# Optimization experiments

Hardware: AMD Instinct MI355X
Metric: run time of the kernel (lower is better)

The kernel has to match this reference:

```python
import jax, jax.numpy as jnp
import numpy as np

M, N, K = 1024, 11008, 4096


def _unpack_i2u(Bp):
    """Unpack 2-bit unsigned weights per decode_i2u_to_i8s interleave.

    Bp: [N, K//4] int8 storage. Within each group of 4 bytes (16 elements),
    output element at position 4*i + j = (byte_j >> (2*i)) & 3.
    Returns [N, K] int8 with values in {0,1,2,3}.
    """
    Bu = jax.lax.bitcast_convert_type(Bp, jnp.uint8)  # [N, K//4]
    n, kc = Bu.shape
    Bg = Bu.reshape(n, kc // 4, 1, 4)                 # [N, G, 1, j]
    shifts = (jnp.arange(4, dtype=jnp.uint8) * jnp.uint8(2)).reshape(1, 1, 4, 1)
    vals = (Bg >> shifts) & jnp.uint8(3)              # [N, G, i, j]
    return vals.reshape(n, kc * 4).astype(jnp.int8)   # [N, K]


def setup_inputs() -> dict:
    key = jax.random.key(0)
    k1, k2 = jax.random.split(key)
    A = jax.random.randint(k1, (M, K), -128, 128, dtype=jnp.int8)
    B = jax.random.randint(k2, (N, K // 4), -128, 128, dtype=jnp.int8)
    return {"A": A, "B": B}


def reference(A, B):
    W = _unpack_i2u(B)  # [N, K] int8
    C = jax.lax.dot_general(
        A, W,
        dimension_numbers=(((1,), (1,)), ((), ())),
        preferred_element_type=jnp.int32,
    )  # [M, N] int32
    return C
```

## Files before the change

### kernel.cpp

```cpp
#include <hip/hip_runtime.h>
#include <stdint.h>


#define MM 1024
#define NN 11008
#define KK 4096
#define MTILES 8
#define NTILES 86
#define NBLOCKS (MTILES * NTILES)
#define STRIDE_A ((size_t)MTILES * 8192)
#define STRIDE_B ((size_t)NTILES * 2048)

using i32x4  = __attribute__((ext_vector_type(4))) int;
using i32x16 = __attribute__((ext_vector_type(16))) int;

__device__ __forceinline__ int pack4(i32x4 v) {
    return (int)(((uint32_t)v[0] & 0xFFu) | (((uint32_t)v[1] & 0xFFu) << 8)
               | (((uint32_t)v[2] & 0xFFu) << 16) | (((uint32_t)v[3] & 0xFFu) << 24));
}

__global__ __launch_bounds__(256) void prep_AB(const int* __restrict__ Asrc,
                                               const int* __restrict__ Bsrc,
                                               uint8_t* __restrict__ A2,
                                               uint8_t* __restrict__ B3) {
    if (blockIdx.x < 1024) {
        const int g = blockIdx.x * 256 + threadIdx.x;
        const int kstep = g >> 12;
        const int rem   = g & 4095;
        const int mtile = rem >> 9;
        const int c     = rem & 511;
        const int row32 = (c >> 7) & 3, kk2 = (c >> 6) & 1;
        const int lane  = c & 63;
        const int row   = mtile * 128 + row32 * 32 + (lane & 31);
        const int kbyte = kstep * 64 + kk2 * 32 + (lane >> 5) * 16;
        const i32x4* s4 = (const i32x4*)(Asrc + (size_t)row * KK + kbyte);
        i32x4 o;
#pragma unroll
        for (int q = 0; q < 4; ++q) o[q] = pack4(s4[q]);
        *(i32x4*)(A2 + (size_t)g * 16) = o;
    } else {
        const int t = (blockIdx.x - 1024) * 256 + threadIdx.x;
        const int n = t >> 6, kstep = t & 63;
        const int ntile = n >> 7, hf = (n >> 6) & 1, ni = (n >> 5) & 1, l31 = n & 31;
        const i32x4* s4 = (const i32x4*)(Bsrc + (size_t)n * (KK / 4) + kstep * 16);
        int w[4];
#pragma unroll
        for (int j = 0; j < 4; ++j) w[j] = pack4(s4[j]);
        uint8_t* base = B3 + ((size_t)kstep * NTILES + ntile) * 2048 + hf * 1024;
        *(int2*)(base + l31 * 16 + ni * 8)        = make_int2(w[0], w[2]);
        *(int2*)(base + (l31 + 32) * 16 + ni * 8) = make_int2(w[1], w[3]);
    }
}

#define GLOAD_LDS16(g, l) __builtin_amdgcn_global_load_lds(                    \
        (const __attribute__((address_space(1))) uint32_t*)(g),                \
        (__attribute__((address_space(3))) uint32_t*)(l), 16, 0, 0)

#define MFMA_I8 __builtin_amdgcn_mfma_i32_32x32x32_i8

#define STAGE(SL, T) do {                                                      \
    const uint8_t* at_ = gA + (size_t)(T) * STRIDE_A;                          \
    uint8_t* l_ = &As[SL][0];                                                  \
    GLOAD_LDS16(at_,        l_ + wave * 1024);                                 \
    GLOAD_LDS16(at_ + 4096, l_ + 4096 + wave * 1024);                          \
    if (wave < 2)                                                              \
        GLOAD_LDS16(gBs + (size_t)(T) * STRIDE_B, l_ + 8192 + wave * 1024);    \
} while (0)

#define COMP(SL) do {                                                          \
    const uint8_t* ab_ = &As[SL][0];                                           \
    i32x4 aA0_ = *(const i32x4*)(ab_ + (wr * 2 + 0) * 2048 + lane * 16);       \
    i32x4 aA1_ = *(const i32x4*)(ab_ + (wr * 2 + 0) * 2048 + 1024 + lane * 16);\
    i32x4 aB0_ = *(const i32x4*)(ab_ + (wr * 2 + 1) * 2048 + lane * 16);       \
    i32x4 aB1_ = *(const i32x4*)(ab_ + (wr * 2 + 1) * 2048 + 1024 + lane * 16);\
    const i32x4 bv_ = *(const i32x4*)(ab_ + 8192 + wc * 1024 + lane * 16);     \
    _Pragma("unroll")                                                          \
    for (int kk2_ = 0; kk2_ < 2; ++kk2_) {                                     \
        const uint32_t q0_ = (uint32_t)bv_[kk2_];                              \
        const uint32_t q1_ = (uint32_t)bv_[2 + kk2_];                          \
        i32x4 b0_, b1_;                                                        \
        _Pragma("unroll")                                                      \
        for (int i_ = 0; i_ < 4; ++i_) {                                       \
            b0_[i_] = (int)((q0_ >> (2 * i_)) & 0x03030303u);                  \
            b1_[i_] = (int)((q1_ >> (2 * i_)) & 0x03030303u);                  \
        }                                                                      \
        const i32x4 am0_ = kk2_ ? aA1_ : aA0_;                                 \
        const i32x4 am1_ = kk2_ ? aB1_ : aB0_;                                 \
        acc[0][0] = MFMA_I8(am0_, b0_, acc[0][0], 0, 0, 0);                    \
        acc[0][1] = MFMA_I8(am0_, b1_, acc[0][1], 0, 0, 0);                    \
        acc[1][0] = MFMA_I8(am1_, b0_, acc[1][0], 0, 0, 0);                    \
        acc[1][1] = MFMA_I8(am1_, b1_, acc[1][1], 0, 0, 0);                    \
    }                                                                          \
} while (0)

#define WAITN(N0, N2) do {                                                     \
    if (wave < 2) asm volatile("s_waitcnt vmcnt(" #N0 ")" ::: "memory");       \
    else          asm volatile("s_waitcnt vmcnt(" #N2 ")" ::: "memory");       \
} while (0)

#define ITER(T, NW0, NW2, DS) do {                                             \
    WAITN(NW0, NW2);                                                           \
    __builtin_amdgcn_s_barrier();                                              \
    __builtin_amdgcn_sched_barrier(0);                                         \
    if (DS) STAGE(((T) + 3) & 3, (T) + 3);                                     \
    COMP((T) & 3);                                                             \
} while (0)

__global__ __launch_bounds__(256, 3) void bitnet_gemm(const uint8_t* __restrict__ A2,
                                                      const uint8_t* __restrict__ B3,
                                                      int* __restrict__ C) {
    const int tid  = threadIdx.x;
    const int lane = tid & 63, wave = tid >> 6;
    const int wr   = wave >> 1, wc = wave & 1;
    const int l31  = lane & 31, h = lane >> 5;

    const int bid = blockIdx.x;
    const int l   = (bid & 7) * (NBLOCKS / 8) + (bid >> 3);
    const int bm  = l & 7;
    const int bn  = l >> 3;

    __shared__ __align__(16) uint8_t As[4][10240];

    const uint8_t* gA  = A2 + (size_t)bm * 8192 + tid * 16;
    const uint8_t* gBs = B3 + (size_t)bn * 2048 + wave * 1024 + lane * 16;

    i32x16 acc[2][2] = {};

    STAGE(0, 0);
    STAGE(1, 1);
    STAGE(2, 2);

#pragma unroll 1
    for (int t = 0; t < 60; t += 4) {
        ITER(t + 0, 6, 4, 1);
        ITER(t + 1, 6, 4, 1);
        ITER(t + 2, 6, 4, 1);
        ITER(t + 3, 6, 4, 1);
    }
    ITER(60, 6, 4, 1);
    ITER(61, 6, 4, 0);
    ITER(62, 3, 2, 0);
    ITER(63, 0, 0, 0);

    const int brow = bm * 128, bcol = bn * 128;
#pragma unroll
    for (int mi = 0; mi < 2; ++mi)
#pragma unroll
        for (int ni = 0; ni < 2; ++ni) {
            const int colg = bcol + wc * 64 + ni * 32 + l31;
#pragma unroll
            for (int r = 0; r < 16; ++r) {
                const int rowin = (r & 3) + 8 * (r >> 2) + 4 * h;
                const int rowg  = brow + wr * 64 + mi * 32 + rowin;
                C[(size_t)rowg * NN + colg] = acc[mi][ni][r];
            }
        }
}

extern "C" void kernel_launch(void* const* d_in, const int* in_sizes, int n_in,
                              void* d_out, int out_size, void* d_ws, size_t ws_size,
                              hipStream_t stream) {
    const int* A32 = (const int*)d_in[0];
    const int* B32 = (const int*)d_in[1];
    int* C = (int*)d_out;

    uint8_t* A2 = (uint8_t*)d_ws;
    uint8_t* B3 = A2 + (size_t)MM * KK;

    prep_AB<<<dim3(1024 + 2752), dim3(256), 0, stream>>>(A32, B32, A2, B3);
    bitnet_gemm<<<dim3(NBLOCKS), dim3(256), 0, stream>>>(A2, B3, C);
}
```

Before: 65.97 us.

## Dedicate a producer wave to global-to-LDS loads, compute waves only run MFMA

Adds a fifth wave per block that issues every global_load_lds transfer for A and B into the 4-slot LDS ring, while the four compute waves just hit barriers and run the dequant plus MFMA loop. This takes vmcnt waits and load issue off the compute waves' critical path, a warp-specialized producer/consumer setup. In exchange the block grows to 320 threads, one wave issues ten loads per step alone, and barrier counts must line up exactly between producer and consumers.

```diff
diff --git a/kernel.cpp b/kernel.cpp
--- a/kernel.cpp
+++ b/kernel.cpp
@@ -58,17 +58,24 @@
 
 #define MFMA_I8 __builtin_amdgcn_mfma_i32_32x32x32_i8
 
-#define STAGE(SL, T) do {                                                      \
+#define PSTAGE(T) do {                                                         \
     const uint8_t* at_ = gA + (size_t)(T) * STRIDE_A;                          \
-    uint8_t* l_ = &As[SL][0];                                                  \
-    GLOAD_LDS16(at_,        l_ + wave * 1024);                                 \
-    GLOAD_LDS16(at_ + 4096, l_ + 4096 + wave * 1024);                          \
-    if (wave < 2)                                                              \
-        GLOAD_LDS16(gBs + (size_t)(T) * STRIDE_B, l_ + 8192 + wave * 1024);    \
+    const uint8_t* bt_ = gB + (size_t)(T) * STRIDE_B;                          \
+    uint8_t* l_ = &As[(T) & 3][0];                                             \
+    GLOAD_LDS16(at_,        l_);                                               \
+    GLOAD_LDS16(at_ + 1024, l_ + 1024);                                        \
+    GLOAD_LDS16(at_ + 2048, l_ + 2048);                                        \
+    GLOAD_LDS16(at_ + 3072, l_ + 3072);                                        \
+    GLOAD_LDS16(at_ + 4096, l_ + 4096);                                        \
+    GLOAD_LDS16(at_ + 5120, l_ + 5120);                                        \
+    GLOAD_LDS16(at_ + 6144, l_ + 6144);                                        \
+    GLOAD_LDS16(at_ + 7168, l_ + 7168);                                        \
+    GLOAD_LDS16(bt_,        l_ + 8192);                                        \
+    GLOAD_LDS16(bt_ + 1024, l_ + 9216);                                        \
 } while (0)
 
-#define COMP(SL) do {                                                          \
-    const uint8_t* ab_ = &As[SL][0];                                           \
+#define COMP(T) do {                                                           \
+    const uint8_t* ab_ = &As[(T) & 3][0];                                      \
     i32x4 aA0_ = *(const i32x4*)(ab_ + (wr * 2 + 0) * 2048 + lane * 16);       \
     i32x4 aA1_ = *(const i32x4*)(ab_ + (wr * 2 + 0) * 2048 + 1024 + lane * 16);\
     i32x4 aB0_ = *(const i32x4*)(ab_ + (wr * 2 + 1) * 2048 + lane * 16);       \
@@ -93,25 +100,14 @@
     }                                                                          \
 } while (0)
 
-#define WAITN(N0, N2) do {                                                     \
-    if (wave < 2) asm volatile("s_waitcnt vmcnt(" #N0 ")" ::: "memory");       \
-    else          asm volatile("s_waitcnt vmcnt(" #N2 ")" ::: "memory");       \
-} while (0)
+#define PWAIT(N) asm volatile("s_waitcnt vmcnt(" #N ")" ::: "memory")
 
-#define ITER(T, NW0, NW2, DS) do {                                             \
-    WAITN(NW0, NW2);                                                           \
-    __builtin_amdgcn_s_barrier();                                              \
-    __builtin_amdgcn_sched_barrier(0);                                         \
-    if (DS) STAGE(((T) + 3) & 3, (T) + 3);                                     \
-    COMP((T) & 3);                                                             \
-} while (0)
-
-__global__ __launch_bounds__(256, 3) void bitnet_gemm(const uint8_t* __restrict__ A2,
+__global__ __launch_bounds__(320, 3) void bitnet_gemm(const uint8_t* __restrict__ A2,
                                                       const uint8_t* __restrict__ B3,
                                                       int* __restrict__ C) {
     const int tid  = threadIdx.x;
     const int lane = tid & 63, wave = tid >> 6;
-    const int wr   = wave >> 1, wc = wave & 1;
+    const int wr   = (wave >> 1) & 1, wc = wave & 1;
     const int l31  = lane & 31, h = lane >> 5;
 
     const int bid = blockIdx.x;
@@ -121,26 +117,43 @@
 
     __shared__ __align__(16) uint8_t As[4][10240];
 
-    const uint8_t* gA  = A2 + (size_t)bm * 8192 + tid * 16;
-    const uint8_t* gBs = B3 + (size_t)bn * 2048 + wave * 1024 + lane * 16;
+    if (wave == 4) {
+        const uint8_t* gA = A2 + (size_t)bm * 8192 + lane * 16;
+        const uint8_t* gB = B3 + (size_t)bn * 2048 + lane * 16;
+
+        PSTAGE(0); PSTAGE(1); PSTAGE(2);
+        PWAIT(20);
+#pragma unroll 1
+        for (int t = 0; t < 60; t += 4) {
+            __builtin_amdgcn_s_barrier(); PSTAGE(t + 3); PWAIT(20);
+            __builtin_amdgcn_s_barrier(); PSTAGE(t + 4); PWAIT(20);
+            __builtin_amdgcn_s_barrier(); PSTAGE(t + 5); PWAIT(20);
+            __builtin_amdgcn_s_barrier(); PSTAGE(t + 6); PWAIT(20);
+        }
+        __builtin_amdgcn_s_barrier(); PSTAGE(63); PWAIT(20);
+        __builtin_amdgcn_s_barrier(); PWAIT(10);
+        __builtin_amdgcn_s_barrier(); PWAIT(0);
+        __builtin_amdgcn_s_barrier();
+        return;
+    }
 
     i32x16 acc[2][2] = {};
 
-    STAGE(0, 0);
-    STAGE(1, 1);
-    STAGE(2, 2);
-
 #pragma unroll 1
-    for (int t = 0; t < 60; t += 4) {
-        ITER(t + 0, 6, 4, 1);
-        ITER(t + 1, 6, 4, 1);
-        ITER(t + 2, 6, 4, 1);
-        ITER(t + 3, 6, 4, 1);
+    for (int t = 0; t < 64; t += 4) {
+        __builtin_amdgcn_s_barrier();
+        __builtin_amdgcn_sched_barrier(0);
+        COMP(t + 0);
+        __builtin_amdgcn_s_barrier();
+        __builtin_amdgcn_sched_barrier(0);
+        COMP(t + 1);
+        __builtin_amdgcn_s_barrier();
+        __builtin_amdgcn_sched_barrier(0);
+        COMP(t + 2);
+        __builtin_amdgcn_s_barrier();
+        __builtin_amdgcn_sched_barrier(0);
+        COMP(t + 3);
     }
-    ITER(60, 6, 4, 1);
-    ITER(61, 6, 4, 0);
-    ITER(62, 3, 2, 0);
-    ITER(63, 0, 0, 0);
 
     const int brow = bm * 128, bcol = bn * 128;
 #pragma unroll
@@ -168,5 +181,5 @@
     uint8_t* B3 = A2 + (size_t)MM * KK;
 
     prep_AB<<<dim3(1024 + 2752), dim3(256), 0, stream>>>(A32, B32, A2, B3);
-    bitnet_gemm<<<dim3(NBLOCKS), dim3(256), 0, stream>>>(A2, B3, C);
+    bitnet_gemm<<<dim3(NBLOCKS), dim3(320), 0, stream>>>(A2, B3, C);
 }
```

After: 63.77 us (median of 3 runs). -3.3%, faster.
